# Optimization experiments

Hardware: AMD Instinct MI355X
Metric: run time of the kernel (lower is better)

The kernel has to match this reference:

```python
import jax, jax.numpy as jnp
import numpy as np

D_MODEL = 1024
N_HEADS = 16
D_K = D_MODEL // N_HEADS
EPS = 1e-6


def setup_inputs() -> dict:
    key = jax.random.key(0)
    ks = jax.random.split(key, 9)
    s = 1.0 / np.sqrt(D_MODEL)
    x = jax.random.normal(ks[0], (4, 4096, D_MODEL), dtype=jnp.float32)
    Wq = jax.random.uniform(ks[1], (D_MODEL, D_MODEL), jnp.float32, -s, s)
    bq = jax.random.uniform(ks[2], (D_MODEL,), jnp.float32, -s, s)
    Wk = jax.random.uniform(ks[3], (D_MODEL, D_MODEL), jnp.float32, -s, s)
    bk = jax.random.uniform(ks[4], (D_MODEL,), jnp.float32, -s, s)
    Wv = jax.random.uniform(ks[5], (D_MODEL, D_MODEL), jnp.float32, -s, s)
    bv = jax.random.uniform(ks[6], (D_MODEL,), jnp.float32, -s, s)
    Wo = jax.random.uniform(ks[7], (D_MODEL, D_MODEL), jnp.float32, -s, s)
    bo = jax.random.uniform(ks[8], (D_MODEL,), jnp.float32, -s, s)
    return {"x": x, "Wq": Wq, "bq": bq, "Wk": Wk, "bk": bk,
            "Wv": Wv, "bv": bv, "Wo": Wo, "bo": bo}


def _feature_map(t):
    # elu(x) + 1
    return jax.nn.elu(t) + 1.0


def reference(x, Wq, bq, Wk, bk, Wv, bv, Wo, bo):
    b, s, _ = x.shape
    # projections, split into heads: [b, h, s, d_k]
    def heads(t):
        return t.reshape(b, s, N_HEADS, D_K).transpose(0, 2, 1, 3)
    q = _feature_map(heads(x @ Wq + bq))
    k = _feature_map(heads(x @ Wk + bk))
    v = heads(x @ Wv + bv)
    # kv accumulation: [b, h, d_k, d_k]
    kv = jnp.einsum('bhsd,bhse->bhde', k, v)
    # normalizer: q . sum_s k  -> [b, h, s, 1]
    z = jnp.einsum('bhsd,bhd->bhs', q, k.sum(axis=2))[..., None]
    out = jnp.einsum('bhsd,bhde->bhse', q, kv) / (z + EPS)
    out = out.transpose(0, 2, 1, 3).reshape(b, s, D_MODEL)
    return out @ Wo + bo
```

## Files before the change

### kernel.cpp

```cpp
#include <hip/hip_runtime.h>


typedef __bf16 bf16;
typedef float  f32x4  __attribute__((ext_vector_type(4)));
typedef short  s16x8  __attribute__((ext_vector_type(8)));
typedef bf16   bf16x4 __attribute__((ext_vector_type(4)));

#define BATCH 4
#define SEQ   4096
#define DM    1024
#define NH    16
#define DK    64
#define MROWS (BATCH*SEQ)
#define EPSV  1e-6f

__device__ __forceinline__ void async_cp16(const bf16* g, bf16* l) {
  __builtin_amdgcn_global_load_lds((const __attribute__((address_space(1))) void*)g,
                                   (__attribute__((address_space(3))) void*)l,
                                   16, 0, 0);
}

__global__ __launch_bounds__(256) void conv_x_kernel(const float* __restrict__ x,
                                                     bf16* __restrict__ xb) {
  int i = (blockIdx.x * 256 + threadIdx.x) * 4;
  float4 f = *reinterpret_cast<const float4*>(x + i);
  bf16x4 o;
  o[0] = (bf16)f.x; o[1] = (bf16)f.y; o[2] = (bf16)f.z; o[3] = (bf16)f.w;
  *reinterpret_cast<bf16x4*>(xb + i) = o;
}

__global__ __launch_bounds__(256) void conv_w_kernel(const float* __restrict__ W0,
                                                     const float* __restrict__ W1,
                                                     const float* __restrict__ W2,
                                                     const float* __restrict__ W3,
                                                     bf16* __restrict__ Wt) {
  __shared__ bf16 tt[64][72];
  const int z = blockIdx.z;
  const float* W = (z == 0) ? W0 : (z == 1) ? W1 : (z == 2) ? W2 : W3;
  const int n0 = blockIdx.x * 64, k0 = blockIdx.y * 64;
  const int tid = threadIdx.x;
#pragma unroll
  for (int i = 0; i < 4; ++i) {
    const int c = tid + i * 256;
    const int krow = c >> 4, nch = c & 15;
    float4 f = *reinterpret_cast<const float4*>(W + (size_t)(k0 + krow) * DM + n0 + nch * 4);
    tt[nch * 4 + 0][krow] = (bf16)f.x;
    tt[nch * 4 + 1][krow] = (bf16)f.y;
    tt[nch * 4 + 2][krow] = (bf16)f.z;
    tt[nch * 4 + 3][krow] = (bf16)f.w;
  }
  __syncthreads();
#pragma unroll
  for (int i = 0; i < 2; ++i) {
    const int c = tid + i * 256;
    const int nrow = c >> 3, kch = c & 7;
    *reinterpret_cast<uint4*>(Wt + (size_t)(z * DM + n0 + nrow) * DM + k0 + kch * 8) =
        *reinterpret_cast<const uint4*>(&tt[nrow][kch * 8]);
  }
}

template <int MODE>
__global__ __launch_bounds__(512, 2) void gemm_bf16(const bf16* __restrict__ A,
                                                    const bf16* __restrict__ Bt,
                                                    void* __restrict__ Cout, int ldc,
                                                    const float* __restrict__ b0,
                                                    const float* __restrict__ b1,
                                                    const float* __restrict__ b2) {
  constexpr int K  = 1024;
  constexpr int BK = 64;
  constexpr int NT = K / BK;
  __shared__ __align__(16) char smem[131072];

  const int tid  = threadIdx.x;
  const int wv   = tid >> 6, lane = tid & 63;
  const int quad = lane >> 4, l16 = lane & 15;
  const int swk  = l16 & 7;

  const int nwg = gridDim.x * gridDim.y;
  int lin = blockIdx.y * gridDim.x + blockIdx.x;
  lin = (lin & 7) * (nwg >> 3) + (lin >> 3);
  const int bm0 = (lin & 63) << 8;
  const int bn0 = (lin >> 6) << 8;

  const int wm = wv >> 2;
  const int wn = wv & 3;

  f32x4 acc[8][4] = {};
  s16x8 af[4][2];
  s16x8 bq[2][2][2];

  const int srow = wv * 8 + (lane >> 3);
  const int scol = ((lane & 7) ^ (lane >> 3)) * 8;
  const bf16* Ag = A  + (size_t)(bm0 + srow) * K + scol;
  const bf16* Bg = Bt + (size_t)(bn0 + srow) * K + scol;
  const int sbase = wv * 1024;

#define STAGE_A(t_, h_) do {                                                   \
    const bf16* g_ = Ag + (size_t)((h_) * 128) * K + (t_) * BK;                \
    char* l_ = smem + ((t_) & 1) * 32768 + (h_) * 16384 + sbase;               \
    async_cp16(g_, (bf16*)l_);                                                 \
    async_cp16(g_ + (size_t)64 * K, (bf16*)(l_ + 8192));                       \
  } while (0)
#define STAGE_B(t_, h_) do {                                                   \
    const bf16* g_ = Bg + (size_t)((h_) * 128) * K + (t_) * BK;                \
    char* l_ = smem + 65536 + ((t_) & 1) * 32768 + (h_) * 16384 + sbase;       \
    async_cp16(g_, (bf16*)l_);                                                 \
    async_cp16(g_ + (size_t)64 * K, (bf16*)(l_ + 8192));                       \
  } while (0)
#define LDA(qm_) do {                                                          \
    const char* ab_ = smem + p * 32768 +                                       \
        (size_t)(wm * 128 + (qm_) * 64 + l16) * 128;                           \
    _Pragma("unroll") for (int mi = 0; mi < 4; ++mi)                           \
      _Pragma("unroll") for (int ks = 0; ks < 2; ++ks)                         \
        af[mi][ks] = *reinterpret_cast<const s16x8*>(                          \
            ab_ + mi * 2048 + (((ks * 4 + quad) ^ swk) << 4));                 \
  } while (0)
#define LDB(qn_) do {                                                          \
    const char* bb_ = smem + 65536 + p * 32768 +                               \
        (size_t)(wn * 64 + (qn_) * 32 + l16) * 128;                            \
    _Pragma("unroll") for (int ni = 0; ni < 2; ++ni)                           \
      _Pragma("unroll") for (int ks = 0; ks < 2; ++ks)                         \
        bq[qn_][ni][ks] = *reinterpret_cast<const s16x8*>(                     \
            bb_ + ni * 2048 + (((ks * 4 + quad) ^ swk) << 4));                 \
  } while (0)
#define MFMA_Q(qm_, qn_) do {                                                  \
    _Pragma("unroll") for (int mi = 0; mi < 4; ++mi)                           \
      _Pragma("unroll") for (int ni = 0; ni < 2; ++ni)                         \
        _Pragma("unroll") for (int ks = 0; ks < 2; ++ks)                       \
          acc[(qm_) * 4 + mi][(qn_) * 2 + ni] =                                \
              __builtin_amdgcn_mfma_f32_16x16x32_bf16(                         \
                  af[mi][ks], bq[qn_][ni][ks],                                 \
                  acc[(qm_) * 4 + mi][(qn_) * 2 + ni], 0, 0, 0);               \
  } while (0)
#define PH_BEGIN() do {                                                        \
    __builtin_amdgcn_s_barrier();                                              \
    asm volatile("s_waitcnt lgkmcnt(0)");                                      \
    __builtin_amdgcn_s_setprio(1);                                             \
  } while (0)
#define PH_END() do {                                                          \
    __builtin_amdgcn_s_setprio(0);                                             \
    __builtin_amdgcn_s_barrier();                                              \
    __builtin_amdgcn_sched_barrier(0);                                         \
  } while (0)

  STAGE_B(0, 0); STAGE_A(0, 0); STAGE_B(0, 1); STAGE_A(0, 1);
  STAGE_B(1, 0); STAGE_A(1, 0);
  asm volatile("s_waitcnt vmcnt(4)");
  __builtin_amdgcn_s_barrier();
  __builtin_amdgcn_sched_barrier(0);

#pragma unroll 2
  for (int t = 0; t < NT; ++t) {
    const int p = t & 1;
    LDA(0); LDB(0);
    if (t + 1 < NT) STAGE_B(t + 1, 1);
    PH_BEGIN(); MFMA_Q(0, 0); PH_END();
    LDB(1);
    if (t + 1 < NT) STAGE_A(t + 1, 1);
    PH_BEGIN(); MFMA_Q(0, 1); PH_END();
    LDA(1);
    if (t + 2 < NT) STAGE_B(t + 2, 0);
    PH_BEGIN(); MFMA_Q(1, 0); PH_END();
    if (t + 2 < NT) STAGE_A(t + 2, 0);
    __builtin_amdgcn_s_barrier();
    asm volatile("s_waitcnt lgkmcnt(0)");
    __builtin_amdgcn_s_setprio(1);
    MFMA_Q(1, 1);
    __builtin_amdgcn_s_setprio(0);
    if (t < NT - 2) asm volatile("s_waitcnt vmcnt(4)");
    else            asm volatile("s_waitcnt vmcnt(0)");
    __builtin_amdgcn_s_barrier();
    __builtin_amdgcn_sched_barrier(0);
  }

  if (MODE == 0) {
    const int part = bn0 >> 10;
    const float* bp = (part == 0) ? b0 : (part == 1) ? b1 : b2;
    bf16* C = (bf16*)Cout;
    bf16 (*Cw)[64] = (bf16(*)[64])(smem + wv * 16384);
#pragma unroll
    for (int ni = 0; ni < 4; ++ni) {
      const int n_l = ni * 16 + l16;
      const float bias = bp[(bn0 + wn * 64 + n_l) & 1023];
#pragma unroll
      for (int mi = 0; mi < 8; ++mi)
#pragma unroll
        for (int r = 0; r < 4; ++r) {
          float v = acc[mi][ni][r] + bias;
          if (part < 2) v = (v > 0.f) ? (v + 1.f) : __expf(v);
          const int row = mi * 16 + quad * 4 + r;
          Cw[row][n_l ^ ((row & 7) << 3)] = (bf16)v;
        }
    }
#pragma unroll
    for (int i = 0; i < 16; ++i) {
      const int row = i * 8 + (lane >> 3), ch = lane & 7;
      *reinterpret_cast<uint4*>(C + (size_t)(bm0 + wm * 128 + row) * ldc +
                                bn0 + wn * 64 + ch * 8) =
          *reinterpret_cast<const uint4*>(&Cw[row][(ch ^ (row & 7)) * 8]);
    }
  } else {
    float* C = (float*)Cout;
    float (*Cwf)[64] = (float(*)[64])(smem + wv * 16384);
#pragma unroll
    for (int h = 0; h < 2; ++h) {
#pragma unroll
      for (int ni = 0; ni < 4; ++ni) {
        const int n_l = ni * 16 + l16;
        const float bias = b0[bn0 + wn * 64 + n_l];
#pragma unroll
        for (int mi = 0; mi < 4; ++mi)
#pragma unroll
          for (int r = 0; r < 4; ++r) {
            const int row = mi * 16 + quad * 4 + r;
            Cwf[row][n_l ^ ((row & 7) << 2)] = acc[h * 4 + mi][ni][r] + bias;
          }
      }
#pragma unroll
      for (int i = 0; i < 16; ++i) {
        const int row = i * 4 + (lane >> 4), ch = lane & 15;
        *reinterpret_cast<float4*>(C + (size_t)(bm0 + wm * 128 + h * 64 + row) * ldc +
                                   bn0 + wn * 64 + ch * 4) =
            *reinterpret_cast<const float4*>(&Cwf[row][(ch ^ (row & 7)) * 4]);
      }
    }
  }
#undef STAGE_A
#undef STAGE_B
#undef LDA
#undef LDB
#undef MFMA_Q
#undef PH_BEGIN
#undef PH_END
}

__global__ __launch_bounds__(256) void kv_ksum_kernel(const bf16* __restrict__ QKV,
                                                      float* __restrict__ kvT,
                                                      float* __restrict__ ksum) {
  __shared__ bf16 Ks[128][64];
  __shared__ bf16 Vs[128][64];
  const int bh = blockIdx.y;
  const int b = bh >> 4, h = bh & 15;
  const int tid = threadIdx.x;
  const int d0 = (tid >> 4) * 4, e0 = (tid & 15) * 4;
  const size_t base = (size_t)b * SEQ * 3072;
  const int colK = 1024 + h * 64, colV = 2048 + h * 64;

  float acc[4][4] = {};
  float ks4[4] = {};

  for (int cc = 0; cc < 4; ++cc) {
    const int s0 = blockIdx.x * 512 + cc * 128;
#pragma unroll
    for (int i = 0; i < 4; ++i) {
      const int c = tid + i * 256;
      const int row = c >> 3, off = (c & 7) * 8;
      const size_t roff = base + (size_t)(s0 + row) * 3072;
      *reinterpret_cast<uint4*>(&Ks[row][off]) =
          *reinterpret_cast<const uint4*>(QKV + roff + colK + off);
      *reinterpret_cast<uint4*>(&Vs[row][off]) =
          *reinterpret_cast<const uint4*>(QKV + roff + colV + off);
    }
    __syncthreads();
#pragma unroll 4
    for (int s = 0; s < 128; ++s) {
      bf16x4 kk = *reinterpret_cast<const bf16x4*>(&Ks[s][d0]);
      bf16x4 vv = *reinterpret_cast<const bf16x4*>(&Vs[s][e0]);
      float kd[4], ve[4];
#pragma unroll
      for (int j = 0; j < 4; ++j) { kd[j] = (float)kk[j]; ve[j] = (float)vv[j]; }
#pragma unroll
      for (int i = 0; i < 4; ++i) {
        ks4[i] += kd[i];
#pragma unroll
        for (int j = 0; j < 4; ++j) acc[i][j] += kd[i] * ve[j];
      }
    }
    __syncthreads();
  }
#pragma unroll
  for (int i = 0; i < 4; ++i)
#pragma unroll
    for (int j = 0; j < 4; ++j)
      atomicAdd(&kvT[(size_t)bh * 4096 + (e0 + j) * 64 + (d0 + i)], acc[i][j]);
  if ((tid & 15) == 0) {
#pragma unroll
    for (int i = 0; i < 4; ++i)
      atomicAdd(&ksum[bh * 64 + d0 + i], ks4[i]);
  }
}

__global__ __launch_bounds__(256) void attn_kernel(const bf16* __restrict__ QKV,
                                                   const float* __restrict__ kvT,
                                                   const float* __restrict__ ksum,
                                                   bf16* __restrict__ ATT) {
  __shared__ bf16 qs[128][72];
  __shared__ bf16 kvs[64][72];
  __shared__ bf16 Ps[128][72];
  __shared__ float zr[128];
  __shared__ float kss[64];
  const int bh = blockIdx.y;
  const int b = bh >> 4, h = bh & 15;
  const int s0 = blockIdx.x * 128;
  const int tid = threadIdx.x, wave = tid >> 6, lane = tid & 63;
  const int quad = lane >> 4, l16 = lane & 15;
  const size_t base = (size_t)b * SEQ * 3072;
  const int colQ = h * 64;

#pragma unroll
  for (int i = 0; i < 4; ++i) {
    const int c = tid + i * 256;
    const int row = c >> 3, off = (c & 7) * 8;
    *reinterpret_cast<uint4*>(&qs[row][off]) =
        *reinterpret_cast<const uint4*>(QKV + base + (size_t)(s0 + row) * 3072 + colQ + off);
  }
  const float* kvg = kvT + (size_t)bh * 4096;
#pragma unroll
  for (int i = 0; i < 4; ++i) {
    const int c = tid + i * 256;
    const int row = c >> 4, off = (c & 15) * 4;
    float4 f = *reinterpret_cast<const float4*>(kvg + row * 64 + off);
    bf16x4 o;
    o[0] = (bf16)f.x; o[1] = (bf16)f.y; o[2] = (bf16)f.z; o[3] = (bf16)f.w;
    *reinterpret_cast<bf16x4*>(&kvs[row][off]) = o;
  }
  if (tid < 64) kss[tid] = ksum[bh * 64 + tid];
  __syncthreads();

  if (tid < 128) {
    float z = 0.f;
#pragma unroll
    for (int d = 0; d < 64; d += 4) {
      bf16x4 q4 = *reinterpret_cast<const bf16x4*>(&qs[tid][d]);
      z += (float)q4[0] * kss[d] + (float)q4[1] * kss[d + 1] +
           (float)q4[2] * kss[d + 2] + (float)q4[3] * kss[d + 3];
    }
    zr[tid] = 1.0f / (z + EPSV);
  }
  __syncthreads();

  const int wn = wave * 32;
  f32x4 pacc[4][2] = {};
#pragma unroll
  for (int ks = 0; ks < 2; ++ks) {
    s16x8 af[4], bf2[2];
#pragma unroll
    for (int mi = 0; mi < 4; ++mi)
      af[mi] = *reinterpret_cast<const s16x8*>(&kvs[mi * 16 + l16][ks * 32 + quad * 8]);
#pragma unroll
    for (int ni = 0; ni < 2; ++ni)
      bf2[ni] = *reinterpret_cast<const s16x8*>(&qs[wn + ni * 16 + l16][ks * 32 + quad * 8]);
#pragma unroll
    for (int mi = 0; mi < 4; ++mi)
#pragma unroll
      for (int ni = 0; ni < 2; ++ni)
        pacc[mi][ni] = __builtin_amdgcn_mfma_f32_16x16x32_bf16(af[mi], bf2[ni],
                                                               pacc[mi][ni], 0, 0, 0);
  }
#pragma unroll
  for (int ni = 0; ni < 2; ++ni) {
    const int s = wn + ni * 16 + l16;
    const float zi = zr[s];
#pragma unroll
    for (int mi = 0; mi < 4; ++mi) {
      bf16x4 o;
#pragma unroll
      for (int r = 0; r < 4; ++r) o[r] = (bf16)(pacc[mi][ni][r] * zi);
      *reinterpret_cast<bf16x4*>(&Ps[s][mi * 16 + quad * 4]) = o;
    }
  }
  __syncthreads();
#pragma unroll
  for (int i = 0; i < 4; ++i) {
    const int c = tid + i * 256;
    const int row = c >> 3, ch = c & 7;
    *reinterpret_cast<uint4*>(ATT + ((size_t)b * SEQ + s0 + row) * DM + h * 64 + ch * 8) =
        *reinterpret_cast<const uint4*>(&Ps[row][ch * 8]);
  }
}

extern "C" void kernel_launch(void* const* d_in, const int* in_sizes, int n_in,
                              void* d_out, int out_size, void* d_ws, size_t ws_size,
                              hipStream_t stream) {
  const float* x  = (const float*)d_in[0];
  const float* Wq = (const float*)d_in[1];
  const float* bq = (const float*)d_in[2];
  const float* Wk = (const float*)d_in[3];
  const float* bk = (const float*)d_in[4];
  const float* Wv = (const float*)d_in[5];
  const float* bv = (const float*)d_in[6];
  const float* Wo = (const float*)d_in[7];
  const float* bo = (const float*)d_in[8];
  float* out = (float*)d_out;

  char* ws = (char*)d_ws;
  bf16*  Xb   = (bf16*)ws;   ws += (size_t)MROWS * DM * 2;
  bf16*  Wt   = (bf16*)ws;   ws += (size_t)4 * DM * DM * 2;
  bf16*  QKV  = (bf16*)ws;   ws += (size_t)MROWS * 3 * DM * 2;
  bf16*  ATT  = (bf16*)ws;   ws += (size_t)MROWS * DM * 2;
  float* kvT  = (float*)ws;  ws += (size_t)64 * 4096 * 4;
  float* ksum = (float*)ws;  ws += (size_t)64 * 64 * 4;

  (void)hipMemsetAsync(kvT, 0, (size_t)64 * 4096 * 4 + (size_t)64 * 64 * 4, stream);

  conv_x_kernel<<<MROWS * DM / 1024, 256, 0, stream>>>(x, Xb);
  conv_w_kernel<<<dim3(16, 16, 4), 256, 0, stream>>>(Wq, Wk, Wv, Wo, Wt);
  gemm_bf16<0><<<dim3(12, 64), 512, 0, stream>>>(Xb, Wt, QKV, 3 * DM, bq, bk, bv);
  kv_ksum_kernel<<<dim3(8, 64), 256, 0, stream>>>(QKV, kvT, ksum);
  attn_kernel<<<dim3(32, 64), 256, 0, stream>>>(QKV, kvT, ksum, ATT);
  gemm_bf16<1><<<dim3(4, 64), 512, 0, stream>>>(ATT, Wt + (size_t)3 * DM * DM, out, DM, bo, bo, bo);
}
```

Measured before the change: 375.0 us.

## Restructure GEMM main loop into two MFMA phases with cross-iteration fragment prefetch

Rewrites the bf16 projection GEMM main loop. The four barrier-delimited MFMA phases per K-tile become two larger phases, and the LDS fragment loads for the next tile are issued at the end of the current iteration. The goal is to cut the number of workgroup barriers per tile and overlap LDS reads and global-to-LDS staging with MFMA work. In exchange, register live ranges get longer, and the reordered staging and barriers must still keep the double-buffered shared memory free of read/write races.

```diff
diff --git a/kernel.cpp b/kernel.cpp
--- a/kernel.cpp
+++ b/kernel.cpp
@@ -107,16 +107,16 @@
     async_cp16(g_, (bf16*)l_);                                                 \
     async_cp16(g_ + (size_t)64 * K, (bf16*)(l_ + 8192));                       \
   } while (0)
-#define LDA(qm_) do {                                                          \
-    const char* ab_ = smem + p * 32768 +                                       \
+#define LDA(pb_, qm_) do {                                                     \
+    const char* ab_ = smem + (pb_) * 32768 +                                   \
         (size_t)(wm * 128 + (qm_) * 64 + l16) * 128;                           \
     _Pragma("unroll") for (int mi = 0; mi < 4; ++mi)                           \
       _Pragma("unroll") for (int ks = 0; ks < 2; ++ks)                         \
         af[mi][ks] = *reinterpret_cast<const s16x8*>(                          \
             ab_ + mi * 2048 + (((ks * 4 + quad) ^ swk) << 4));                 \
   } while (0)
-#define LDB(qn_) do {                                                          \
-    const char* bb_ = smem + 65536 + p * 32768 +                               \
+#define LDB(pb_, qn_) do {                                                     \
+    const char* bb_ = smem + 65536 + (pb_) * 32768 +                           \
         (size_t)(wn * 64 + (qn_) * 32 + l16) * 128;                            \
     _Pragma("unroll") for (int ni = 0; ni < 2; ++ni)                           \
       _Pragma("unroll") for (int ks = 0; ks < 2; ++ks)                         \
@@ -132,45 +132,43 @@
                   af[mi][ks], bq[qn_][ni][ks],                                 \
                   acc[(qm_) * 4 + mi][(qn_) * 2 + ni], 0, 0, 0);               \
   } while (0)
-#define PH_BEGIN() do {                                                        \
-    __builtin_amdgcn_s_barrier();                                              \
-    asm volatile("s_waitcnt lgkmcnt(0)");                                      \
-    __builtin_amdgcn_s_setprio(1);                                             \
-  } while (0)
-#define PH_END() do {                                                          \
-    __builtin_amdgcn_s_setprio(0);                                             \
-    __builtin_amdgcn_s_barrier();                                              \
-    __builtin_amdgcn_sched_barrier(0);                                         \
-  } while (0)
 
   STAGE_B(0, 0); STAGE_A(0, 0); STAGE_B(0, 1); STAGE_A(0, 1);
   STAGE_B(1, 0); STAGE_A(1, 0);
   asm volatile("s_waitcnt vmcnt(4)");
   __builtin_amdgcn_s_barrier();
   __builtin_amdgcn_sched_barrier(0);
+  LDA(0, 0); LDB(0, 0); LDB(0, 1);
+  __builtin_amdgcn_sched_barrier(0);
 
 #pragma unroll 2
   for (int t = 0; t < NT; ++t) {
     const int p = t & 1;
-    LDA(0); LDB(0);
     if (t + 1 < NT) STAGE_B(t + 1, 1);
-    PH_BEGIN(); MFMA_Q(0, 0); PH_END();
-    LDB(1);
+    asm volatile("s_waitcnt lgkmcnt(0)");
+    __builtin_amdgcn_sched_barrier(0);
+    __builtin_amdgcn_s_setprio(1);
+    MFMA_Q(0, 0); MFMA_Q(0, 1);
+    __builtin_amdgcn_s_setprio(0);
+    LDA(p, 1);
+    __builtin_amdgcn_sched_barrier(0);
     if (t + 1 < NT) STAGE_A(t + 1, 1);
-    PH_BEGIN(); MFMA_Q(0, 1); PH_END();
-    LDA(1);
-    if (t + 2 < NT) STAGE_B(t + 2, 0);
-    PH_BEGIN(); MFMA_Q(1, 0); PH_END();
-    if (t + 2 < NT) STAGE_A(t + 2, 0);
-    __builtin_amdgcn_s_barrier();
     asm volatile("s_waitcnt lgkmcnt(0)");
+    __builtin_amdgcn_sched_barrier(0);
     __builtin_amdgcn_s_setprio(1);
-    MFMA_Q(1, 1);
+    MFMA_Q(1, 0); MFMA_Q(1, 1);
     __builtin_amdgcn_s_setprio(0);
-    if (t < NT - 2) asm volatile("s_waitcnt vmcnt(4)");
-    else            asm volatile("s_waitcnt vmcnt(0)");
     __builtin_amdgcn_s_barrier();
     __builtin_amdgcn_sched_barrier(0);
+    if (t + 2 < NT) { STAGE_B(t + 2, 0); STAGE_A(t + 2, 0); }
+    if (t + 1 < NT) {
+      if (t + 2 < NT) asm volatile("s_waitcnt vmcnt(4)");
+      else            asm volatile("s_waitcnt vmcnt(0)");
+      __builtin_amdgcn_s_barrier();
+      __builtin_amdgcn_sched_barrier(0);
+      LDA(p ^ 1, 0); LDB(p ^ 1, 0); LDB(p ^ 1, 1);
+      __builtin_amdgcn_sched_barrier(0);
+    }
   }
 
   if (MODE == 0) {
@@ -230,8 +228,6 @@
 #undef LDA
 #undef LDB
 #undef MFMA_Q
-#undef PH_BEGIN
-#undef PH_END
 }
 
 __global__ __launch_bounds__(256) void kv_ksum_kernel(const bf16* __restrict__ QKV,
```

New measurement: 370.9 us. About the same (-1.1%).
